# Kernel tuning notes

Measured on AMD Instinct MI355X. Metric: run time of the kernel, lower is better.

## Reference

```python
import jax, jax.numpy as jnp
import numpy as np

B, T, D = 4, 2048, 768
E, F, K = 8, 4 * 768, 2


def setup_inputs() -> dict:
    key = jax.random.key(0)
    ks = jax.random.split(key, 5)
    s = 0.02
    return {
        "x": jax.random.normal(ks[0], (B, T, D), dtype=jnp.float32),
        "Wg": jax.random.normal(ks[1], (D, E), dtype=jnp.float32) * s,
        "bg": jnp.zeros((E,), dtype=jnp.float32),
        "W1": jax.random.normal(ks[2], (E, D, F), dtype=jnp.float32) * s,
        "b1": jnp.zeros((E, F), dtype=jnp.float32),
        "W2": jax.random.normal(ks[3], (E, F, D), dtype=jnp.float32) * s,
        "b2": jnp.zeros((E, D), dtype=jnp.float32),
    }


def reference(x, Wg, bg, W1, b1, W2, b2):
    b, t, d = x.shape
    x_flat = x.reshape(-1, d)                      # [N, D]
    n = x_flat.shape[0]

    # Router: softmax over expert logits, take top-2
    gates = jax.nn.softmax(x_flat @ Wg + bg, axis=-1)   # [N, E]
    topk_g, topk_i = jax.lax.top_k(gates, K)            # [N, K]

    # Combine weights: zero for non-selected experts -> math identical to
    # masked dispatch in the torch loop (out = sum_k gate_k * expert_{idx_k}(x))
    combine = jnp.zeros((n, W1.shape[0]), dtype=gates.dtype)
    combine = combine.at[jnp.arange(n)[:, None], topk_i].add(topk_g)  # [N, E]

    # Per-expert MLP applied densely, then weighted combine (zero weights
    # kill non-selected experts' contributions)
    h = jnp.einsum('nd,edf->enf', x_flat, W1) + b1[:, None, :]  # [E, N, F]
    h = jax.nn.gelu(h, approximate=False)                        # torch nn.GELU = exact
    y = jnp.einsum('enf,efd->end', h, W2) + b2[:, None, :]       # [E, N, D]
    out = jnp.einsum('ne,end->nd', combine, y)                   # [N, D]
    return out.reshape(b, t, d)
```

## Files before the change

kernel.cpp:

```cpp
#include <hip/hip_runtime.h>
#include <hip/hip_bf16.h>


#define N_TOK 8192
#define D_DIM 768
#define E_EXP 8
#define F_DIM 3072
#define CAP   8192
#define NT_MAX 136

typedef __attribute__((ext_vector_type(8))) short s8v;
typedef __attribute__((ext_vector_type(4))) float f4v;
typedef unsigned short u16;
typedef unsigned int   u32;
typedef unsigned long long u64;

static __device__ __forceinline__ u16 f2bf(float f) {
    u32 u = __float_as_uint(f);
    return (u16)((u + 0x7fffu + ((u >> 16) & 1u)) >> 16);
}
static __device__ __forceinline__ float bf2f(u16 v) {
    return __uint_as_float((u32)v << 16);
}
static __device__ __forceinline__ float gelu_exact(float v) {
    return 0.5f * v * (1.0f + erff(v * 0.70710678118654752440f));
}
static __device__ __forceinline__ void gld_lds16(const u16* g, u16* l) {
    __builtin_amdgcn_global_load_lds(
        (const __attribute__((address_space(1))) void*)g,
        (__attribute__((address_space(3))) void*)l, 16, 0, 0);
}

__device__ __forceinline__ void pack_w_body(
    const float* __restrict__ src, u16* __restrict__ dst,
    int rt, int kc, int e, int K1, int M2, int KC, int TR, int ntm)
{
    __shared__ float ls[64][132];
    const float* se = src + (size_t)e * K1 * M2;
    const int tid = threadIdx.x;

    const int kr = tid >> 2, mq = tid & 3;
    const float* srow = se + (size_t)(kc * 64 + kr) * M2 + rt * 128 + mq * 32;
    #pragma unroll
    for (int it = 0; it < 8; ++it)
        *(float4*)&ls[kr][mq * 32 + it * 4] = *(const float4*)(srow + it * 4);
    __syncthreads();

    u16* dt_ = dst + ((size_t)(e * ntm + (rt * 128) / TR) * KC + kc) * ((size_t)TR * 64)
                   + (size_t)((rt * 128) % TR) * 64;
    const int rr = tid >> 1, hf = tid & 1;
    #pragma unroll
    for (int j = 0; j < 4; ++j) {
        const int c8 = hf * 4 + j;
        union { s8v v; u16 u[8]; } o;
        #pragma unroll
        for (int jj = 0; jj < 8; ++jj) o.u[jj] = f2bf(ls[c8 * 8 + jj][rr]);
        *(s8v*)&dt_[rr * 64 + ((c8 ^ (rr & 7)) * 8)] = o.v;
    }
}

__global__ __launch_bounds__(256) void prep_kernel(
    const float* __restrict__ x, const float* __restrict__ Wg,
    const float* __restrict__ bg, const float* __restrict__ W1,
    const float* __restrict__ W2, u32* __restrict__ rec_idx,
    float2* __restrict__ rec_g, u16* __restrict__ w1g,
    u16* __restrict__ w2g, int* __restrict__ counts)
{
    const int bid = blockIdx.x;
    if (bid == 0 && threadIdx.x < E_EXP) counts[threadIdx.x] = 0;

    if (bid < 2048) {
        const int wave = threadIdx.x >> 6;
        const int lane = threadIdx.x & 63;
        const int t = bid * 4 + wave;

        float acc[8];
        #pragma unroll
        for (int e = 0; e < 8; ++e) acc[e] = 0.f;

        const float* xrow = x + (size_t)t * D_DIM + lane * 12;
        #pragma unroll
        for (int i = 0; i < 3; ++i) {
            float4 xv = *(const float4*)(xrow + i * 4);
            float xs[4] = {xv.x, xv.y, xv.z, xv.w};
            #pragma unroll
            for (int j = 0; j < 4; ++j) {
                const int d = lane * 12 + i * 4 + j;
                const float4 w0 = *(const float4*)(Wg + (size_t)d * 8);
                const float4 w1 = *(const float4*)(Wg + (size_t)d * 8 + 4);
                acc[0] += xs[j] * w0.x;  acc[1] += xs[j] * w0.y;
                acc[2] += xs[j] * w0.z;  acc[3] += xs[j] * w0.w;
                acc[4] += xs[j] * w1.x;  acc[5] += xs[j] * w1.y;
                acc[6] += xs[j] * w1.z;  acc[7] += xs[j] * w1.w;
            }
        }
        #pragma unroll
        for (int e = 0; e < 8; ++e) {
            float v = acc[e];
            #pragma unroll
            for (int off = 32; off > 0; off >>= 1) v += __shfl_xor(v, off, 64);
            acc[e] = v + bg[e];
        }
        if (lane == 0) {
            float mx = acc[0];
            #pragma unroll
            for (int e = 1; e < 8; ++e) mx = fmaxf(mx, acc[e]);
            float p[8], s = 0.f;
            #pragma unroll
            for (int e = 0; e < 8; ++e) { p[e] = expf(acc[e] - mx); s += p[e]; }
            const float inv = 1.f / s;
            #pragma unroll
            for (int e = 0; e < 8; ++e) p[e] *= inv;

            int i0 = 0; float g0 = p[0];
            #pragma unroll
            for (int e = 1; e < 8; ++e) if (p[e] > g0) { g0 = p[e]; i0 = e; }
            int i1 = -1; float g1 = -1.f;
            #pragma unroll
            for (int e = 0; e < 8; ++e) if (e != i0 && p[e] > g1) { g1 = p[e]; i1 = e; }

            rec_idx[t] = (u32)i0 | ((u32)i1 << 4);
            rec_g[t] = make_float2(g0, g1);
        }
    } else if (bid < 4352) {
        const int id = bid - 2048;
        const int e = id / 288, rem = id - e * 288;
        const int rt = rem / 12, kc = rem - rt * 12;
        pack_w_body(W1, w1g, rt, kc, e, D_DIM, F_DIM, 12, 256, 12);
    } else {
        const int id = bid - 4352;
        const int e = id / 288, rem = id - e * 288;
        const int rt = rem / 48, kc = rem - rt * 48;
        pack_w_body(W2, w2g, rt, kc, e, F_DIM, D_DIM, 48, 128, 6);
    }
}

__global__ __launch_bounds__(256) void moe_scatter(
    const u32* __restrict__ rec_idx, const float2* __restrict__ rec_g,
    int* __restrict__ counts, int* __restrict__ tokbuf,
    float* __restrict__ gatebuf)
{
    const int t = blockIdx.x * 256 + threadIdx.x;
    const int lane = threadIdx.x & 63;
    const u32 pk = rec_idx[t];
    const int i0 = pk & 15, i1 = (pk >> 4) & 15;
    const float2 g = rec_g[t];
    const u64 lmask = ((u64)1 << lane) - 1;

    #pragma unroll
    for (int e = 0; e < 8; ++e) {
        const u64 m0 = __ballot(i0 == e);
        const u64 m1 = __ballot(i1 == e);
        const int c0 = __popcll(m0);
        const int total = c0 + __popcll(m1);
        if (total > 0) {
            int base = 0;
            if (lane == 0) base = atomicAdd(&counts[e], total);
            base = __shfl(base, 0, 64);
            if (i0 == e) {
                const int p = base + __popcll(m0 & lmask);
                tokbuf[(size_t)e * CAP + p] = 2 * t;
                gatebuf[(size_t)e * CAP + p] = g.x;
            }
            if (i1 == e) {
                const int p = base + c0 + __popcll(m1 & lmask);
                tokbuf[(size_t)e * CAP + p] = 2 * t + 1;
                gatebuf[(size_t)e * CAP + p] = g.y;
            }
        }
    }
}

__global__ void scan_kernel(const int* __restrict__ counts,
                            int* __restrict__ te, int* __restrict__ tb,
                            int* __restrict__ ntile) {
    if (threadIdx.x == 0) {
        int nt = 0;
        for (int e = 0; e < E_EXP; ++e)
            for (int k = 0; k * 128 < counts[e]; ++k) {
                te[nt] = e; tb[nt] = k * 128; ++nt;
            }
        *ntile = nt;
    }
}

__global__ __launch_bounds__(256) void pack_x(
    const float* __restrict__ x, const int* __restrict__ counts,
    const int* __restrict__ te, const int* __restrict__ tb,
    const int* __restrict__ ntile, const int* __restrict__ tokbuf,
    u16* __restrict__ xg)
{
    const int bx = blockIdx.x, kc = blockIdx.y;
    if (bx >= *ntile) return;
    const int e = te[bx], base = tb[bx], cnt = counts[e];
    const int tid = threadIdx.x;
    const int r = tid >> 1, hf = tid & 1;
    int ent = base + r; if (ent >= cnt) ent = cnt - 1;
    const int tok = tokbuf[(size_t)e * CAP + ent] >> 1;
    const float* xr = x + (size_t)tok * D_DIM + kc * 64 + hf * 32;
    u16* xt = xg + ((size_t)bx * 12 + kc) * 8192 + r * 64;
    #pragma unroll
    for (int j = 0; j < 4; ++j) {
        float4 a = *(const float4*)(xr + j * 8);
        float4 b = *(const float4*)(xr + j * 8 + 4);
        union { s8v v; u16 u[8]; } o;
        o.u[0] = f2bf(a.x); o.u[1] = f2bf(a.y); o.u[2] = f2bf(a.z); o.u[3] = f2bf(a.w);
        o.u[4] = f2bf(b.x); o.u[5] = f2bf(b.y); o.u[6] = f2bf(b.z); o.u[7] = f2bf(b.w);
        *(s8v*)&xt[((hf * 4 + j) ^ (r & 7)) * 8] = o.v;
    }
}

__global__ __launch_bounds__(256, 2) void s1_gemm(
    const u16* __restrict__ xg, const u16* __restrict__ w1g,
    const float* __restrict__ b1, const int* __restrict__ te,
    const int* __restrict__ ntile, u16* __restrict__ hg)
{
    __shared__ u16 Als[16384];
    __shared__ u16 Bls[8192];
    const int bx = blockIdx.x, by = blockIdx.y;
    if (bx >= *ntile) return;
    const int e = te[bx];

    const int tid  = threadIdx.x;
    const int w    = tid >> 6;
    const int lane = tid & 63;
    const int wm   = w & 1, wn = w >> 1;
    const int q    = lane >> 4, ln = lane & 15;

    const u16* Ap = w1g + ((size_t)(e * 12 + by) * 12) * 16384 + w * 4096 + lane * 8;
    const u16* Bp = xg  + ((size_t)bx * 12) * 8192 + w * 2048 + lane * 8;

    f4v acc[8][4];
    #pragma unroll
    for (int mi = 0; mi < 8; ++mi)
        #pragma unroll
        for (int ni = 0; ni < 4; ++ni) acc[mi][ni] = (f4v){0.f,0.f,0.f,0.f};

    for (int s = 0; s < 12; ++s) {
        __syncthreads();
        #pragma unroll
        for (int it = 0; it < 8; ++it)
            gld_lds16(Ap + it * 512, &Als[w * 4096 + it * 512]);
        #pragma unroll
        for (int it = 0; it < 4; ++it)
            gld_lds16(Bp + it * 512, &Bls[w * 2048 + it * 512]);
        Ap += 16384; Bp += 8192;
        __syncthreads();
        #pragma unroll
        for (int kk = 0; kk < 2; ++kk) {
            const int col = ((kk * 4 + q) ^ (ln & 7)) * 8;
            s8v af[8], bf[4];
            #pragma unroll
            for (int mi = 0; mi < 8; ++mi)
                af[mi] = *(const s8v*)&Als[(wm * 128 + mi * 16 + ln) * 64 + col];
            #pragma unroll
            for (int ni = 0; ni < 4; ++ni)
                bf[ni] = *(const s8v*)&Bls[(wn * 64 + ni * 16 + ln) * 64 + col];
            #pragma unroll
            for (int mi = 0; mi < 8; ++mi)
                #pragma unroll
                for (int ni = 0; ni < 4; ++ni)
                    acc[mi][ni] = __builtin_amdgcn_mfma_f32_16x16x32_bf16(
                        af[mi], bf[ni], acc[mi][ni], 0, 0, 0);
        }
    }

    const float* b1e = b1 + (size_t)e * F_DIM + by * 256;
    #pragma unroll
    for (int mi = 0; mi < 8; ++mi) {
        const int floc = wm * 128 + mi * 16 + q * 4;
        const int kc   = by * 4 + wm * 2 + (mi >> 2);
        const int c8   = (mi & 3) * 2 + (q >> 1);
        const float4 bv = *(const float4*)&b1e[floc];
        u16* ht = hg + ((size_t)bx * 48 + kc) * 8192;
        #pragma unroll
        for (int ni = 0; ni < 4; ++ni) {
            const int rr = wn * 64 + ni * 16 + ln;
            u16 us[4];
            us[0] = f2bf(gelu_exact(acc[mi][ni][0] + bv.x));
            us[1] = f2bf(gelu_exact(acc[mi][ni][1] + bv.y));
            us[2] = f2bf(gelu_exact(acc[mi][ni][2] + bv.z));
            us[3] = f2bf(gelu_exact(acc[mi][ni][3] + bv.w));
            uint2 pk;
            pk.x = (u32)us[0] | ((u32)us[1] << 16);
            pk.y = (u32)us[2] | ((u32)us[3] << 16);
            *(uint2*)&hg[((size_t)bx * 48 + kc) * 8192 +
                         rr * 64 + ((c8 ^ (rr & 7)) * 8) + (q & 1) * 4] = pk;
        }
        (void)ht;
    }
}

__global__ __launch_bounds__(256) void s2_gemm(
    const u16* __restrict__ hg, const u16* __restrict__ w2g,
    const int* __restrict__ counts, const int* __restrict__ te,
    const int* __restrict__ tb, const int* __restrict__ ntile,
    const int* __restrict__ tokbuf, const float* __restrict__ gatebuf,
    u16* __restrict__ y)
{
    __shared__ u16 Als[8192];
    __shared__ u16 Bls[8192];
    __shared__ int   sts[128];
    __shared__ float sg[128];
    const int bx = blockIdx.x, by = blockIdx.y;
    if (bx >= *ntile) return;
    const int e = te[bx], base = tb[bx], cnt = counts[e];

    const int tid  = threadIdx.x;
    const int w    = tid >> 6;
    const int lane = tid & 63;
    const int wm   = w & 1, wn = w >> 1;
    const int q    = lane >> 4, ln = lane & 15;

    if (tid < 128) {
        const int ent = base + tid;
        const bool v = ent < cnt;
        sts[tid] = v ? tokbuf[(size_t)e * CAP + ent] : -1;
        sg[tid]  = v ? gatebuf[(size_t)e * CAP + ent] : 0.f;
    }

    const u16* Ap = w2g + ((size_t)(e * 6 + by) * 48) * 8192 + w * 2048 + lane * 8;
    const u16* Bp = hg  + ((size_t)bx * 48) * 8192 + w * 2048 + lane * 8;

    f4v acc[4][4];
    #pragma unroll
    for (int mi = 0; mi < 4; ++mi)
        #pragma unroll
        for (int ni = 0; ni < 4; ++ni) acc[mi][ni] = (f4v){0.f,0.f,0.f,0.f};

    for (int s = 0; s < 48; ++s) {
        __syncthreads();
        #pragma unroll
        for (int it = 0; it < 4; ++it) {
            gld_lds16(Ap + it * 512, &Als[w * 2048 + it * 512]);
            gld_lds16(Bp + it * 512, &Bls[w * 2048 + it * 512]);
        }
        Ap += 8192; Bp += 8192;
        __syncthreads();
        #pragma unroll
        for (int kk = 0; kk < 2; ++kk) {
            const int col = ((kk * 4 + q) ^ (ln & 7)) * 8;
            s8v af[4], bf[4];
            #pragma unroll
            for (int mi = 0; mi < 4; ++mi)
                af[mi] = *(const s8v*)&Als[(wm * 64 + mi * 16 + ln) * 64 + col];
            #pragma unroll
            for (int ni = 0; ni < 4; ++ni)
                bf[ni] = *(const s8v*)&Bls[(wn * 64 + ni * 16 + ln) * 64 + col];
            #pragma unroll
            for (int mi = 0; mi < 4; ++mi)
                #pragma unroll
                for (int ni = 0; ni < 4; ++ni)
                    acc[mi][ni] = __builtin_amdgcn_mfma_f32_16x16x32_bf16(
                        af[mi], bf[ni], acc[mi][ni], 0, 0, 0);
        }
    }

    #pragma unroll
    for (int ni = 0; ni < 4; ++ni) {
        const int rr = wn * 64 + ni * 16 + ln;
        const int ts = sts[rr];
        if (ts >= 0) {
            const float g = sg[rr];
            u16* yr = y + (size_t)ts * D_DIM + by * 128 + wm * 64;
            #pragma unroll
            for (int mi = 0; mi < 4; ++mi) {
                u16 us[4];
                us[0] = f2bf(g * acc[mi][ni][0]);
                us[1] = f2bf(g * acc[mi][ni][1]);
                us[2] = f2bf(g * acc[mi][ni][2]);
                us[3] = f2bf(g * acc[mi][ni][3]);
                uint2 pk;
                pk.x = (u32)us[0] | ((u32)us[1] << 16);
                pk.y = (u32)us[2] | ((u32)us[3] << 16);
                *(uint2*)&yr[mi * 16 + q * 4] = pk;
            }
        }
    }
}

__global__ __launch_bounds__(256) void combine_kernel(
    const u16* __restrict__ y, const u32* __restrict__ rec_idx,
    const float2* __restrict__ rec_g, const float* __restrict__ b2,
    float* __restrict__ out)
{
    const int gid = blockIdx.x * 256 + threadIdx.x;
    const int t = gid / 192;
    const int c = (gid - t * 192) * 4;
    const u32 pk = rec_idx[t];
    const int i0 = pk & 15, i1 = (pk >> 4) & 15;
    const float2 g = rec_g[t];
    union { uint2 p; u16 u[4]; } a, b;
    a.p = *(const uint2*)&y[(size_t)(2 * t) * D_DIM + c];
    b.p = *(const uint2*)&y[(size_t)(2 * t + 1) * D_DIM + c];
    const float4 ba = *(const float4*)&b2[(size_t)i0 * D_DIM + c];
    const float4 bb = *(const float4*)&b2[(size_t)i1 * D_DIM + c];
    float4 o;
    o.x = g.x * ba.x + g.y * bb.x + bf2f(a.u[0]) + bf2f(b.u[0]);
    o.y = g.x * ba.y + g.y * bb.y + bf2f(a.u[1]) + bf2f(b.u[1]);
    o.z = g.x * ba.z + g.y * bb.z + bf2f(a.u[2]) + bf2f(b.u[2]);
    o.w = g.x * ba.w + g.y * bb.w + bf2f(a.u[3]) + bf2f(b.u[3]);
    *(float4*)&out[(size_t)t * D_DIM + c] = o;
}

extern "C" void kernel_launch(void* const* d_in, const int* in_sizes, int n_in,
                              void* d_out, int out_size, void* d_ws, size_t ws_size,
                              hipStream_t stream) {
    const float* x  = (const float*)d_in[0];
    const float* Wg = (const float*)d_in[1];
    const float* bg = (const float*)d_in[2];
    const float* W1 = (const float*)d_in[3];
    const float* b1 = (const float*)d_in[4];
    const float* W2 = (const float*)d_in[5];
    const float* b2 = (const float*)d_in[6];
    float* out = (float*)d_out;

    char* ws = (char*)d_ws;
    size_t off = 0;
    u16* xg  = (u16*)(ws + off); off += (size_t)NT_MAX * 12 * 8192 * sizeof(u16);
    u16* w1g = (u16*)(ws + off); off += (size_t)E_EXP * F_DIM * D_DIM * sizeof(u16);
    u16* w2g = (u16*)(ws + off); off += (size_t)E_EXP * D_DIM * F_DIM * sizeof(u16);
    u16* hg  = (u16*)(ws + off); off += (size_t)NT_MAX * 48 * 8192 * sizeof(u16);
    u16* y   = (u16*)(ws + off); off += (size_t)2 * N_TOK * D_DIM * sizeof(u16);
    int* tokbuf = (int*)(ws + off);      off += (size_t)E_EXP * CAP * sizeof(int);
    float* gatebuf = (float*)(ws + off); off += (size_t)E_EXP * CAP * sizeof(float);
    u32* rec_idx = (u32*)(ws + off);     off += (size_t)N_TOK * sizeof(u32);
    float2* rec_g = (float2*)(ws + off); off += (size_t)N_TOK * sizeof(float2);
    int* counts = (int*)(ws + off);      off += 64;
    int* te     = (int*)(ws + off);      off += NT_MAX * sizeof(int);
    int* tb     = (int*)(ws + off);      off += NT_MAX * sizeof(int);
    int* ntile  = (int*)(ws + off);      off += 64;

    prep_kernel<<<6656, 256, 0, stream>>>(x, Wg, bg, W1, W2, rec_idx, rec_g,
                                          w1g, w2g, counts);
    moe_scatter<<<N_TOK / 256, 256, 0, stream>>>(rec_idx, rec_g, counts, tokbuf, gatebuf);
    scan_kernel<<<1, 64, 0, stream>>>(counts, te, tb, ntile);
    pack_x<<<dim3(NT_MAX, 12), 256, 0, stream>>>(x, counts, te, tb, ntile, tokbuf, xg);

    s1_gemm<<<dim3(NT_MAX, 12), 256, 0, stream>>>(xg, w1g, b1, te, ntile, hg);
    s2_gemm<<<dim3(NT_MAX, 6), 256, 0, stream>>>(hg, w2g, counts, te, tb, ntile,
                                                 tokbuf, gatebuf, y);
    combine_kernel<<<(N_TOK * 192) / 256, 256, 0, stream>>>(y, rec_idx, rec_g, b2, out);
}
```

Measured before the change: 533.3 us.

## Double-buffer GEMM LDS tiles with 32-wide K chunks and use fast GELU

Repacks the bf16 weight, x and hidden tiles into K chunks of 32 with a new XOR swizzle. Both expert GEMMs now double-buffer LDS, prefetching the next chunk while MFMAs run on the current one, with one barrier per iteration. The exact erf GELU is replaced by an Abramowitz-Stegun polynomial using hardware rcp and exp2, which cuts epilogue cost at a small accuracy price. The loop now has twice as many iterations, each doing less work.

```diff
diff --git a/kernel.cpp b/kernel.cpp
--- a/kernel.cpp
+++ b/kernel.cpp
@@ -22,8 +22,18 @@
 static __device__ __forceinline__ float bf2f(u16 v) {
     return __uint_as_float((u32)v << 16);
 }
-static __device__ __forceinline__ float gelu_exact(float v) {
-    return 0.5f * v * (1.0f + erff(v * 0.70710678118654752440f));
+static __device__ __forceinline__ float gelu_fast(float v) {
+    const float av = fabsf(v);
+    const float z  = av * 0.70710678118654752440f;
+    const float t  = __builtin_amdgcn_rcpf(fmaf(0.3275911f, z, 1.0f));
+    const float w  = __builtin_amdgcn_exp2f(-z * z * 1.4426950408889634f);
+    float p = fmaf(1.061405429f, t, -1.453152027f);
+    p = fmaf(p, t,  1.421413741f);
+    p = fmaf(p, t, -0.284496736f);
+    p = fmaf(p, t,  0.254829592f);
+    p = p * t;
+    const float E = 1.0f - p * w;
+    return 0.5f * (v + av * E);
 }
 static __device__ __forceinline__ void gld_lds16(const u16* g, u16* l) {
     __builtin_amdgcn_global_load_lds(
@@ -33,29 +43,32 @@
 
 __device__ __forceinline__ void pack_w_body(
     const float* __restrict__ src, u16* __restrict__ dst,
-    int rt, int kc, int e, int K1, int M2, int KC, int TR, int ntm)
+    int rt, int kc64, int e, int K1, int M2, int KC2, int TR, int ntm)
 {
     __shared__ float ls[64][132];
     const float* se = src + (size_t)e * K1 * M2;
     const int tid = threadIdx.x;
 
     const int kr = tid >> 2, mq = tid & 3;
-    const float* srow = se + (size_t)(kc * 64 + kr) * M2 + rt * 128 + mq * 32;
+    const float* srow = se + (size_t)(kc64 * 64 + kr) * M2 + rt * 128 + mq * 32;
     #pragma unroll
     for (int it = 0; it < 8; ++it)
         *(float4*)&ls[kr][mq * 32 + it * 4] = *(const float4*)(srow + it * 4);
     __syncthreads();
 
-    u16* dt_ = dst + ((size_t)(e * ntm + (rt * 128) / TR) * KC + kc) * ((size_t)TR * 64)
-                   + (size_t)((rt * 128) % TR) * 64;
+    u16* dt_ = dst + ((size_t)(e * ntm + (rt * 128) / TR) * KC2 + kc64 * 2)
+                     * ((size_t)TR * 32)
+                   + (size_t)((rt * 128) % TR) * 32;
     const int rr = tid >> 1, hf = tid & 1;
+    u16* dc = dt_ + (size_t)hf * TR * 32;
+    const int row = ((rt * 128) % TR) + rr;
     #pragma unroll
     for (int j = 0; j < 4; ++j) {
-        const int c8 = hf * 4 + j;
         union { s8v v; u16 u[8]; } o;
         #pragma unroll
-        for (int jj = 0; jj < 8; ++jj) o.u[jj] = f2bf(ls[c8 * 8 + jj][rr]);
-        *(s8v*)&dt_[rr * 64 + ((c8 ^ (rr & 7)) * 8)] = o.v;
+        for (int jj = 0; jj < 8; ++jj)
+            o.u[jj] = f2bf(ls[hf * 32 + j * 8 + jj][rr]);
+        *(s8v*)&dc[(size_t)rr * 32 + ((j ^ ((row >> 1) & 3)) * 8)] = o.v;
     }
 }
 
@@ -126,12 +139,12 @@
         const int id = bid - 2048;
         const int e = id / 288, rem = id - e * 288;
         const int rt = rem / 12, kc = rem - rt * 12;
-        pack_w_body(W1, w1g, rt, kc, e, D_DIM, F_DIM, 12, 256, 12);
+        pack_w_body(W1, w1g, rt, kc, e, D_DIM, F_DIM, 24, 256, 12);
     } else {
         const int id = bid - 4352;
         const int e = id / 288, rem = id - e * 288;
         const int rt = rem / 48, kc = rem - rt * 48;
-        pack_w_body(W2, w2g, rt, kc, e, F_DIM, D_DIM, 48, 128, 6);
+        pack_w_body(W2, w2g, rt, kc, e, F_DIM, D_DIM, 96, 128, 6);
     }
 }
 
@@ -198,7 +211,7 @@
     int ent = base + r; if (ent >= cnt) ent = cnt - 1;
     const int tok = tokbuf[(size_t)e * CAP + ent] >> 1;
     const float* xr = x + (size_t)tok * D_DIM + kc * 64 + hf * 32;
-    u16* xt = xg + ((size_t)bx * 12 + kc) * 8192 + r * 64;
+    u16* xt = xg + ((size_t)bx * 24 + kc * 2 + hf) * 4096;
     #pragma unroll
     for (int j = 0; j < 4; ++j) {
         float4 a = *(const float4*)(xr + j * 8);
@@ -206,7 +219,7 @@
         union { s8v v; u16 u[8]; } o;
         o.u[0] = f2bf(a.x); o.u[1] = f2bf(a.y); o.u[2] = f2bf(a.z); o.u[3] = f2bf(a.w);
         o.u[4] = f2bf(b.x); o.u[5] = f2bf(b.y); o.u[6] = f2bf(b.z); o.u[7] = f2bf(b.w);
-        *(s8v*)&xt[((hf * 4 + j) ^ (r & 7)) * 8] = o.v;
+        *(s8v*)&xt[(size_t)r * 32 + ((j ^ ((r >> 1) & 3)) * 8)] = o.v;
     }
 }
 
@@ -215,8 +228,8 @@
     const float* __restrict__ b1, const int* __restrict__ te,
     const int* __restrict__ ntile, u16* __restrict__ hg)
 {
-    __shared__ u16 Als[16384];
-    __shared__ u16 Bls[8192];
+    __shared__ u16 Als[2][8192];
+    __shared__ u16 Bls[2][4096];
     const int bx = blockIdx.x, by = blockIdx.y;
     if (bx >= *ntile) return;
     const int e = te[bx];
@@ -226,9 +239,10 @@
     const int lane = tid & 63;
     const int wm   = w & 1, wn = w >> 1;
     const int q    = lane >> 4, ln = lane & 15;
-
-    const u16* Ap = w1g + ((size_t)(e * 12 + by) * 12) * 16384 + w * 4096 + lane * 8;
-    const u16* Bp = xg  + ((size_t)bx * 12) * 8192 + w * 2048 + lane * 8;
+    const int colU = (q ^ ((ln >> 1) & 3)) * 8;
+
+    const u16* Ab = w1g + (size_t)(e * 12 + by) * 24 * 8192;
+    const u16* Bb = xg  + (size_t)bx * 24 * 4096;
 
     f4v acc[8][4];
     #pragma unroll
@@ -236,58 +250,69 @@
         #pragma unroll
         for (int ni = 0; ni < 4; ++ni) acc[mi][ni] = (f4v){0.f,0.f,0.f,0.f};
 
-    for (int s = 0; s < 12; ++s) {
+    {
+        const u16* A0 = Ab + w * 2048 + lane * 8;
+        const u16* B0 = Bb + w * 1024 + lane * 8;
+        #pragma unroll
+        for (int it = 0; it < 4; ++it)
+            gld_lds16(A0 + it * 512, &Als[0][w * 2048 + it * 512]);
+        #pragma unroll
+        for (int it = 0; it < 2; ++it)
+            gld_lds16(B0 + it * 512, &Bls[0][w * 1024 + it * 512]);
+    }
+    __syncthreads();
+
+    for (int s = 0; s < 24; ++s) {
+        const int nxt = s + 1;
+        if (nxt < 24) {
+            const u16* An = Ab + (size_t)nxt * 8192 + w * 2048 + lane * 8;
+            const u16* Bn = Bb + (size_t)nxt * 4096 + w * 1024 + lane * 8;
+            u16* Ad = &Als[nxt & 1][w * 2048];
+            u16* Bd = &Bls[nxt & 1][w * 1024];
+            #pragma unroll
+            for (int it = 0; it < 4; ++it) gld_lds16(An + it * 512, Ad + it * 512);
+            #pragma unroll
+            for (int it = 0; it < 2; ++it) gld_lds16(Bn + it * 512, Bd + it * 512);
+        }
+        const int cur = s & 1;
+        s8v af[8], bf[4];
+        #pragma unroll
+        for (int mi = 0; mi < 8; ++mi)
+            af[mi] = *(const s8v*)&Als[cur][(wm * 128 + mi * 16 + ln) * 32 + colU];
+        #pragma unroll
+        for (int ni = 0; ni < 4; ++ni)
+            bf[ni] = *(const s8v*)&Bls[cur][(wn * 64 + ni * 16 + ln) * 32 + colU];
+        #pragma unroll
+        for (int mi = 0; mi < 8; ++mi)
+            #pragma unroll
+            for (int ni = 0; ni < 4; ++ni)
+                acc[mi][ni] = __builtin_amdgcn_mfma_f32_16x16x32_bf16(
+                    af[mi], bf[ni], acc[mi][ni], 0, 0, 0);
         __syncthreads();
-        #pragma unroll
-        for (int it = 0; it < 8; ++it)
-            gld_lds16(Ap + it * 512, &Als[w * 4096 + it * 512]);
-        #pragma unroll
-        for (int it = 0; it < 4; ++it)
-            gld_lds16(Bp + it * 512, &Bls[w * 2048 + it * 512]);
-        Ap += 16384; Bp += 8192;
-        __syncthreads();
-        #pragma unroll
-        for (int kk = 0; kk < 2; ++kk) {
-            const int col = ((kk * 4 + q) ^ (ln & 7)) * 8;
-            s8v af[8], bf[4];
-            #pragma unroll
-            for (int mi = 0; mi < 8; ++mi)
-                af[mi] = *(const s8v*)&Als[(wm * 128 + mi * 16 + ln) * 64 + col];
-            #pragma unroll
-            for (int ni = 0; ni < 4; ++ni)
-                bf[ni] = *(const s8v*)&Bls[(wn * 64 + ni * 16 + ln) * 64 + col];
-            #pragma unroll
-            for (int mi = 0; mi < 8; ++mi)
-                #pragma unroll
-                for (int ni = 0; ni < 4; ++ni)
-                    acc[mi][ni] = __builtin_amdgcn_mfma_f32_16x16x32_bf16(
-                        af[mi], bf[ni], acc[mi][ni], 0, 0, 0);
-        }
     }
 
     const float* b1e = b1 + (size_t)e * F_DIM + by * 256;
     #pragma unroll
     for (int mi = 0; mi < 8; ++mi) {
         const int floc = wm * 128 + mi * 16 + q * 4;
-        const int kc   = by * 4 + wm * 2 + (mi >> 2);
-        const int c8   = (mi & 3) * 2 + (q >> 1);
+        const int kc2  = by * 8 + (floc >> 5);
+        const int cg   = (floc >> 3) & 3;
         const float4 bv = *(const float4*)&b1e[floc];
-        u16* ht = hg + ((size_t)bx * 48 + kc) * 8192;
         #pragma unroll
         for (int ni = 0; ni < 4; ++ni) {
             const int rr = wn * 64 + ni * 16 + ln;
             u16 us[4];
-            us[0] = f2bf(gelu_exact(acc[mi][ni][0] + bv.x));
-            us[1] = f2bf(gelu_exact(acc[mi][ni][1] + bv.y));
-            us[2] = f2bf(gelu_exact(acc[mi][ni][2] + bv.z));
-            us[3] = f2bf(gelu_exact(acc[mi][ni][3] + bv.w));
+            us[0] = f2bf(gelu_fast(acc[mi][ni][0] + bv.x));
+            us[1] = f2bf(gelu_fast(acc[mi][ni][1] + bv.y));
+            us[2] = f2bf(gelu_fast(acc[mi][ni][2] + bv.z));
+            us[3] = f2bf(gelu_fast(acc[mi][ni][3] + bv.w));
             uint2 pk;
             pk.x = (u32)us[0] | ((u32)us[1] << 16);
             pk.y = (u32)us[2] | ((u32)us[3] << 16);
-            *(uint2*)&hg[((size_t)bx * 48 + kc) * 8192 +
-                         rr * 64 + ((c8 ^ (rr & 7)) * 8) + (q & 1) * 4] = pk;
-        }
-        (void)ht;
+            *(uint2*)&hg[((size_t)bx * 96 + kc2) * 4096 +
+                         (size_t)rr * 32 + ((cg ^ ((rr >> 1) & 3)) * 8) +
+                         (q & 1) * 4] = pk;
+        }
     }
 }
 
@@ -298,8 +323,8 @@
     const int* __restrict__ tokbuf, const float* __restrict__ gatebuf,
     u16* __restrict__ y)
 {
-    __shared__ u16 Als[8192];
-    __shared__ u16 Bls[8192];
+    __shared__ u16 Als[2][4096];
+    __shared__ u16 Bls[2][4096];
     __shared__ int   sts[128];
     __shared__ float sg[128];
     const int bx = blockIdx.x, by = blockIdx.y;
@@ -311,6 +336,7 @@
     const int lane = tid & 63;
     const int wm   = w & 1, wn = w >> 1;
     const int q    = lane >> 4, ln = lane & 15;
+    const int colU = (q ^ ((ln >> 1) & 3)) * 8;
 
     if (tid < 128) {
         const int ent = base + tid;
@@ -319,8 +345,8 @@
         sg[tid]  = v ? gatebuf[(size_t)e * CAP + ent] : 0.f;
     }
 
-    const u16* Ap = w2g + ((size_t)(e * 6 + by) * 48) * 8192 + w * 2048 + lane * 8;
-    const u16* Bp = hg  + ((size_t)bx * 48) * 8192 + w * 2048 + lane * 8;
+    const u16* Ab = w2g + (size_t)(e * 6 + by) * 96 * 4096;
+    const u16* Bb = hg  + (size_t)bx * 96 * 4096;
 
     f4v acc[4][4];
     #pragma unroll
@@ -328,32 +354,43 @@
         #pragma unroll
         for (int ni = 0; ni < 4; ++ni) acc[mi][ni] = (f4v){0.f,0.f,0.f,0.f};
 
-    for (int s = 0; s < 48; ++s) {
+    {
+        const u16* A0 = Ab + w * 1024 + lane * 8;
+        const u16* B0 = Bb + w * 1024 + lane * 8;
+        gld_lds16(A0,       &Als[0][w * 1024]);
+        gld_lds16(A0 + 512, &Als[0][w * 1024 + 512]);
+        gld_lds16(B0,       &Bls[0][w * 1024]);
+        gld_lds16(B0 + 512, &Bls[0][w * 1024 + 512]);
+    }
+    __syncthreads();
+
+    for (int s = 0; s < 96; ++s) {
+        const int nxt = s + 1;
+        if (nxt < 96) {
+            const u16* An = Ab + (size_t)nxt * 4096 + w * 1024 + lane * 8;
+            const u16* Bn = Bb + (size_t)nxt * 4096 + w * 1024 + lane * 8;
+            u16* Ad = &Als[nxt & 1][w * 1024];
+            u16* Bd = &Bls[nxt & 1][w * 1024];
+            gld_lds16(An,       Ad);
+            gld_lds16(An + 512, Ad + 512);
+            gld_lds16(Bn,       Bd);
+            gld_lds16(Bn + 512, Bd + 512);
+        }
+        const int cur = s & 1;
+        s8v af[4], bf[4];
+        #pragma unroll
+        for (int mi = 0; mi < 4; ++mi)
+            af[mi] = *(const s8v*)&Als[cur][(wm * 64 + mi * 16 + ln) * 32 + colU];
+        #pragma unroll
+        for (int ni = 0; ni < 4; ++ni)
+            bf[ni] = *(const s8v*)&Bls[cur][(wn * 64 + ni * 16 + ln) * 32 + colU];
+        #pragma unroll
+        for (int mi = 0; mi < 4; ++mi)
+            #pragma unroll
+            for (int ni = 0; ni < 4; ++ni)
+                acc[mi][ni] = __builtin_amdgcn_mfma_f32_16x16x32_bf16(
+                    af[mi], bf[ni], acc[mi][ni], 0, 0, 0);
         __syncthreads();
-        #pragma unroll
-        for (int it = 0; it < 4; ++it) {
-            gld_lds16(Ap + it * 512, &Als[w * 2048 + it * 512]);
-            gld_lds16(Bp + it * 512, &Bls[w * 2048 + it * 512]);
-        }
-        Ap += 8192; Bp += 8192;
-        __syncthreads();
-        #pragma unroll
-        for (int kk = 0; kk < 2; ++kk) {
-            const int col = ((kk * 4 + q) ^ (ln & 7)) * 8;
-            s8v af[4], bf[4];
-            #pragma unroll
-            for (int mi = 0; mi < 4; ++mi)
-                af[mi] = *(const s8v*)&Als[(wm * 64 + mi * 16 + ln) * 64 + col];
-            #pragma unroll
-            for (int ni = 0; ni < 4; ++ni)
-                bf[ni] = *(const s8v*)&Bls[(wn * 64 + ni * 16 + ln) * 64 + col];
-            #pragma unroll
-            for (int mi = 0; mi < 4; ++mi)
-                #pragma unroll
-                for (int ni = 0; ni < 4; ++ni)
-                    acc[mi][ni] = __builtin_amdgcn_mfma_f32_16x16x32_bf16(
-                        af[mi], bf[ni], acc[mi][ni], 0, 0, 0);
-        }
     }
 
     #pragma unroll
@@ -417,10 +454,10 @@
 
     char* ws = (char*)d_ws;
     size_t off = 0;
-    u16* xg  = (u16*)(ws + off); off += (size_t)NT_MAX * 12 * 8192 * sizeof(u16);
+    u16* xg  = (u16*)(ws + off); off += (size_t)NT_MAX * 24 * 4096 * sizeof(u16);
     u16* w1g = (u16*)(ws + off); off += (size_t)E_EXP * F_DIM * D_DIM * sizeof(u16);
     u16* w2g = (u16*)(ws + off); off += (size_t)E_EXP * D_DIM * F_DIM * sizeof(u16);
-    u16* hg  = (u16*)(ws + off); off += (size_t)NT_MAX * 48 * 8192 * sizeof(u16);
+    u16* hg  = (u16*)(ws + off); off += (size_t)NT_MAX * 96 * 4096 * sizeof(u16);
     u16* y   = (u16*)(ws + off); off += (size_t)2 * N_TOK * D_DIM * sizeof(u16);
     int* tokbuf = (int*)(ws + off);      off += (size_t)E_EXP * CAP * sizeof(int);
     float* gatebuf = (float*)(ws + off); off += (size_t)E_EXP * CAP * sizeof(float);
```

New measurement: 529.7 us. Within noise of the previous version (-0.7%).
